# Kernel tuning notes

Measured on AMD Instinct MI355X. Metric: run time of the kernel, lower is better.

## Reference

```python
import jax, jax.numpy as jnp
import numpy as np

XN = 144
YN = 144
BN_EPS = 1e-5


def setup_inputs() -> dict:
    key = jax.random.key(0)
    k1, k2, k3, k4, k5 = jax.random.split(key, 5)
    B, P, M, F, C = 8, 12000, 32, 9, 64
    pillars = jax.random.normal(k1, (B, P, M, F), dtype=jnp.float32)
    pillar_indices = jax.random.randint(k2, (B, P, 3), 0, 144, dtype=jnp.int64)
    conv_w = jax.random.normal(k3, (C, F), dtype=jnp.float32) * 0.1  # 1x1 conv, no bias
    bn_gamma = jnp.ones((C,), dtype=jnp.float32)
    bn_beta = jnp.zeros((C,), dtype=jnp.float32)
    bn_mean = jax.random.normal(k4, (C,), dtype=jnp.float32) * 0.01
    bn_var = jax.random.uniform(k5, (C,), dtype=jnp.float32, minval=0.5, maxval=1.5)
    return {"pillars": pillars, "pillar_indices": pillar_indices, "conv_w": conv_w,
            "bn_gamma": bn_gamma, "bn_beta": bn_beta, "bn_mean": bn_mean, "bn_var": bn_var}


def reference(pillars, pillar_indices, conv_w, bn_gamma, bn_beta, bn_mean, bn_var):
    # pillars: [B, P, M, F] -> 1x1 conv over feature dim -> [B, C, P, M]
    x = jnp.einsum('bpmf,cf->bcpm', pillars, conv_w)
    # BatchNorm2d (inference) + ReLU
    inv_std = jax.lax.rsqrt(bn_var + BN_EPS)
    x = (x - bn_mean[None, :, None, None]) * (bn_gamma * inv_std)[None, :, None, None] \
        + bn_beta[None, :, None, None]
    x = jax.nn.relu(x)
    # MaxPool2d((1, M)): max over points-per-pillar axis -> [B, C, P]
    feat = jnp.max(x, axis=-1)
    # Scatter pillar features into BEV canvas [C, Xn*Yn]
    y_idx = pillar_indices[:, :, 1]                      # [B, P]
    x_idx = jnp.clip(pillar_indices[:, :, 2], 0, 143)    # [B, P]
    flat_idx = y_idx * XN + x_idx                        # [B, P]

    C = feat.shape[1]

    def scatter_one(f, idx):  # f: [C, P], idx: [P]
        canvas = jnp.zeros((C, XN * YN), dtype=f.dtype)
        return canvas.at[:, idx].set(f)

    out = jax.vmap(scatter_one)(feat, flat_idx)          # [B, C, Xn*Yn]
    return out.reshape(feat.shape[0], C, XN, YN)
```

## Files before the change

### kernel.cpp

```cpp
#include <hip/hip_runtime.h>
#include <hip/hip_bf16.h>
#include <stdint.h>

#define NB 8
#define NP 12000
#define NM 32
#define NF 9
#define NC 64
#define NX 144
#define NCELL (144*144)

#define PPW 8
#define FEAT_WAVES ((NB*NP)/PPW)
#define FEAT_BLOCKS (FEAT_WAVES/4)

typedef __attribute__((ext_vector_type(8)))  short bfrag8;
typedef __attribute__((ext_vector_type(16))) float accf16;
typedef float f32x4u __attribute__((ext_vector_type(4), aligned(4)));

#define WS_BTAB  0
#define WS_SHIFT 2048
#define WS_WIN   4096
#define WS_FEAT  668672
#define WS_NEED  (WS_FEAT + (size_t)NB*NP*NC*4)

__global__ void winner_prep_kernel(const int* __restrict__ idx, int* __restrict__ winner,
                                   const float* __restrict__ conv_w,
                                   const float* __restrict__ gamma,
                                   const float* __restrict__ beta,
                                   const float* __restrict__ mean,
                                   const float* __restrict__ var,
                                   unsigned short* __restrict__ btab,
                                   float* __restrict__ shift)
{
    int t = blockIdx.x * blockDim.x + threadIdx.x;
    if (t < NB * NP) {
        int b = t / NP;
        int p = t - b * NP;
        int y = idx[t * 3 + 1];
        int x = idx[t * 3 + 2];
        x = x < 0 ? 0 : (x > 143 ? 143 : x);
        y = y < 0 ? 0 : (y > 143 ? 143 : y);
        atomicMax(&winner[b * NCELL + y * NX + x], p);
    }
    if (blockIdx.x == 0) {
        int tt = threadIdx.x;
        if (tt < 128) {
            int ct = tt >> 6, L = tt & 63;
            int c  = ct * 32 + (L & 31);
            int kq = L >> 5;
            float sc = gamma[c] * rsqrtf(var[c] + 1e-5f);
            unsigned short* dst = btab + (ct * 64 + L) * 8;
            #pragma unroll
            for (int j = 0; j < 8; ++j) {
                int k = kq * 8 + j;
                float w = (k < NF) ? conv_w[c * NF + k] * sc : 0.f;
                __hip_bfloat16 h = __float2bfloat16(w);
                dst[j] = *(unsigned short*)&h;
            }
        }
        if (tt < NC) {
            float sc = gamma[tt] * rsqrtf(var[tt] + 1e-5f);
            shift[tt] = beta[tt] - mean[tt] * sc;
        }
    }
}

__device__ __forceinline__ float max16(const accf16& a) {
    float t0 = fmaxf(fmaxf(a[0], a[1]),  fmaxf(a[2], a[3]));
    float t1 = fmaxf(fmaxf(a[4], a[5]),  fmaxf(a[6], a[7]));
    float t2 = fmaxf(fmaxf(a[8], a[9]),  fmaxf(a[10], a[11]));
    float t3 = fmaxf(fmaxf(a[12], a[13]), fmaxf(a[14], a[15]));
    return fmaxf(fmaxf(t0, t1), fmaxf(t2, t3));
}

template <bool COMPACT>
__global__ void __launch_bounds__(256) feat_dense_kernel(
    const float* __restrict__ pillars,
    const unsigned short* __restrict__ btab,
    const float* __restrict__ shift,
    const int*   __restrict__ idx,
    const int*   __restrict__ winner,
    float* __restrict__ feat_ws,
    float* __restrict__ out)
{
    int tid  = threadIdx.x;
    int lane = tid & 63;
    int wave = blockIdx.x * 4 + (tid >> 6);
    int row  = lane & 31;
    int kq   = lane >> 5;

    bfrag8 b0 = *(const bfrag8*)(btab + lane * 8);
    bfrag8 b1 = *(const bfrag8*)(btab + (64 + lane) * 8);
    float  sh = shift[lane];
    accf16 z  = {};

    const float* wbase = pillars + (size_t)wave * (PPW * NM * NF) + row * NF;

    #pragma unroll
    for (int g = 0; g < PPW / 4; ++g) {
        f32x4u lo[4], hi[4];
        float  e8[4];
        #pragma unroll
        for (int i = 0; i < 4; ++i) {
            const float* base = wbase + (size_t)(g * 4 + i) * (NM * NF);
            lo[i] = *(const f32x4u*)(base);
            hi[i] = *(const f32x4u*)(base + 4);
            e8[i] = base[8];
        }
        #pragma unroll
        for (int i = 0; i < 4; ++i) {
            int pil = wave * PPW + g * 4 + i;
            float s[8];
            s[0] = kq ? e8[i] : lo[i][0];
            s[1] = kq ? 0.f   : lo[i][1];
            s[2] = kq ? 0.f   : lo[i][2];
            s[3] = kq ? 0.f   : lo[i][3];
            s[4] = kq ? 0.f   : hi[i][0];
            s[5] = kq ? 0.f   : hi[i][1];
            s[6] = kq ? 0.f   : hi[i][2];
            s[7] = kq ? 0.f   : hi[i][3];
            bfrag8 a;
            #pragma unroll
            for (int j = 0; j < 8; ++j) {
                __hip_bfloat16 h = __float2bfloat16(s[j]);
                a[j] = *(short*)&h;
            }
            accf16 acc0 = __builtin_amdgcn_mfma_f32_32x32x16_bf16(a, b0, z, 0, 0, 0);
            accf16 acc1 = __builtin_amdgcn_mfma_f32_32x32x16_bf16(a, b1, z, 0, 0, 0);

            float v0 = max16(acc0);
            float v1 = max16(acc1);
            v0 = fmaxf(v0, __shfl_xor(v0, 32));
            v1 = fmaxf(v1, __shfl_xor(v1, 32));
            float r = (lane < 32) ? v0 : v1;
            r += sh;
            r = r > 0.f ? r : 0.f;

            if (COMPACT) {
                feat_ws[(size_t)pil * NC + lane] = r;
            } else {
                int b = pil / NP, p = pil - b * NP;
                int y = idx[pil * 3 + 1], x = idx[pil * 3 + 2];
                x = x < 0 ? 0 : (x > 143 ? 143 : x);
                y = y < 0 ? 0 : (y > 143 ? 143 : y);
                int cell = y * NX + x;
                if (winner[b * NCELL + cell] == p)
                    out[((size_t)(b * NC + lane)) * NCELL + cell] = r;
            }
        }
    }
}

__global__ void __launch_bounds__(256) scatter_kernel(
    const int* __restrict__ winner,
    const float* __restrict__ feat_ws,
    float* __restrict__ out)
{
    int t  = blockIdx.x * blockDim.x + threadIdx.x;
    int c4 = t % (NCELL / 4);
    int bq = t / (NCELL / 4);
    int q  = bq & 3;
    int b  = bq >> 2;
    int cellbase = c4 * 4;

    int4 wv = *(const int4*)(winner + b * NCELL + cellbase);
    long long base0 = wv.x < 0 ? -1 : ((long long)(b * NP + wv.x)) * NC;
    long long base1 = wv.y < 0 ? -1 : ((long long)(b * NP + wv.y)) * NC;
    long long base2 = wv.z < 0 ? -1 : ((long long)(b * NP + wv.z)) * NC;
    long long base3 = wv.w < 0 ? -1 : ((long long)(b * NP + wv.w)) * NC;

    const float4 zf = make_float4(0.f, 0.f, 0.f, 0.f);
    #pragma unroll
    for (int k = 0; k < 4; ++k) {
        int c0 = q * 16 + k * 4;
        float4 f0 = base0 < 0 ? zf : *(const float4*)(feat_ws + base0 + c0);
        float4 f1 = base1 < 0 ? zf : *(const float4*)(feat_ws + base1 + c0);
        float4 f2 = base2 < 0 ? zf : *(const float4*)(feat_ws + base2 + c0);
        float4 f3 = base3 < 0 ? zf : *(const float4*)(feat_ws + base3 + c0);
        float* o = out + ((size_t)(b * NC + c0)) * NCELL + cellbase;
        *(float4*)(o + 0ULL * NCELL) = make_float4(f0.x, f1.x, f2.x, f3.x);
        *(float4*)(o + 1ULL * NCELL) = make_float4(f0.y, f1.y, f2.y, f3.y);
        *(float4*)(o + 2ULL * NCELL) = make_float4(f0.z, f1.z, f2.z, f3.z);
        *(float4*)(o + 3ULL * NCELL) = make_float4(f0.w, f1.w, f2.w, f3.w);
    }
}

extern "C" void kernel_launch(void* const* d_in, const int* in_sizes, int n_in,
                              void* d_out, int out_size, void* d_ws, size_t ws_size,
                              hipStream_t stream) {
    const float* pillars = (const float*)d_in[0];
    const int*   idx     = (const int*)d_in[1];
    const float* conv_w  = (const float*)d_in[2];
    const float* gamma   = (const float*)d_in[3];
    const float* beta    = (const float*)d_in[4];
    const float* mean    = (const float*)d_in[5];
    const float* var     = (const float*)d_in[6];
    float* out = (float*)d_out;

    char* ws = (char*)d_ws;
    unsigned short* btab    = (unsigned short*)(ws + WS_BTAB);
    float*          shift   = (float*)(ws + WS_SHIFT);
    int*            winner  = (int*)(ws + WS_WIN);
    float*          feat_ws = (float*)(ws + WS_FEAT);

    const bool compact = ws_size >= WS_NEED;

    hipMemsetAsync(winner, 0xFF, (size_t)NB * NCELL * sizeof(int), stream);
    winner_prep_kernel<<<(NB * NP + 255) / 256, 256, 0, stream>>>(
        idx, winner, conv_w, gamma, beta, mean, var, btab, shift);

    if (compact) {
        feat_dense_kernel<true><<<FEAT_BLOCKS, 256, 0, stream>>>(
            pillars, btab, shift, idx, winner, feat_ws, out);
        int sthreads = NB * 4 * (NCELL / 4);
        scatter_kernel<<<sthreads / 256, 256, 0, stream>>>(winner, feat_ws, out);
    } else {
        hipMemsetAsync(out, 0, (size_t)out_size * sizeof(float), stream);
        feat_dense_kernel<false><<<FEAT_BLOCKS, 256, 0, stream>>>(
            pillars, btab, shift, idx, winner, feat_ws, out);
    }
}
```

Before: 210.3 us.

## Store winner features in cell-major workspace and transpose via LDS in scatter

The feature kernel now writes only winning pillars' features, directly into a cell-indexed [B, cell, C] workspace instead of a pillar-indexed one. The winner check and cell index are hoisted to the start of each wave. The scatter kernel reads contiguous 64-cell tiles, transposes them through shared memory and writes coalesced rows of the [B, C, cell] output. This replaces the scattered gather by pillar id with streaming reads, at the cost of a larger workspace (cells x channels) and a possible fallback to the non-compact path if the workspace is too small.

```diff
diff --git a/kernel.cpp b/kernel.cpp
--- a/kernel.cpp
+++ b/kernel.cpp
@@ -13,6 +13,7 @@
 #define PPW 8
 #define FEAT_WAVES ((NB*NP)/PPW)
 #define FEAT_BLOCKS (FEAT_WAVES/4)
+#define TILES_PER_B (NCELL/64)
 
 typedef __attribute__((ext_vector_type(8)))  short bfrag8;
 typedef __attribute__((ext_vector_type(16))) float accf16;
@@ -21,8 +22,8 @@
 #define WS_BTAB  0
 #define WS_SHIFT 2048
 #define WS_WIN   4096
-#define WS_FEAT  668672
-#define WS_NEED  (WS_FEAT + (size_t)NB*NP*NC*4)
+#define WS_CELL  667648
+#define WS_NEED  (WS_CELL + (size_t)NB*NCELL*NC*4)
 
 __global__ void winner_prep_kernel(const int* __restrict__ idx, int* __restrict__ winner,
                                    const float* __restrict__ conv_w,
@@ -81,7 +82,7 @@
     const float* __restrict__ shift,
     const int*   __restrict__ idx,
     const int*   __restrict__ winner,
-    float* __restrict__ feat_ws,
+    float* __restrict__ feat_cell,
     float* __restrict__ out)
 {
     int tid  = threadIdx.x;
@@ -89,11 +90,26 @@
     int wave = blockIdx.x * 4 + (tid >> 6);
     int row  = lane & 31;
     int kq   = lane >> 5;
+    int b    = wave / (NP / PPW);
 
     bfrag8 b0 = *(const bfrag8*)(btab + lane * 8);
     bfrag8 b1 = *(const bfrag8*)(btab + (64 + lane) * 8);
     float  sh = shift[lane];
     accf16 z  = {};
+
+    int cellv[PPW];
+    bool winv[PPW];
+    #pragma unroll
+    for (int i = 0; i < PPW; ++i) {
+        int pil = wave * PPW + i;
+        int y = idx[pil * 3 + 1];
+        int x = idx[pil * 3 + 2];
+        x = x < 0 ? 0 : (x > 143 ? 143 : x);
+        y = y < 0 ? 0 : (y > 143 ? 143 : y);
+        int cell = y * NX + x;
+        cellv[i] = cell;
+        winv[i]  = (winner[b * NCELL + cell] == pil - b * NP);
+    }
 
     const float* wbase = pillars + (size_t)wave * (PPW * NM * NF) + row * NF;
 
@@ -110,7 +126,7 @@
         }
         #pragma unroll
         for (int i = 0; i < 4; ++i) {
-            int pil = wave * PPW + g * 4 + i;
+            int pi = g * 4 + i;
             float s[8];
             s[0] = kq ? e8[i] : lo[i][0];
             s[1] = kq ? 0.f   : lo[i][1];
@@ -137,52 +153,53 @@
             r += sh;
             r = r > 0.f ? r : 0.f;
 
-            if (COMPACT) {
-                feat_ws[(size_t)pil * NC + lane] = r;
-            } else {
-                int b = pil / NP, p = pil - b * NP;
-                int y = idx[pil * 3 + 1], x = idx[pil * 3 + 2];
-                x = x < 0 ? 0 : (x > 143 ? 143 : x);
-                y = y < 0 ? 0 : (y > 143 ? 143 : y);
-                int cell = y * NX + x;
-                if (winner[b * NCELL + cell] == p)
-                    out[((size_t)(b * NC + lane)) * NCELL + cell] = r;
+            if (winv[pi]) {
+                if (COMPACT) {
+                    feat_cell[((size_t)(b * NCELL + cellv[pi])) * NC + lane] = r;
+                } else {
+                    out[((size_t)(b * NC + lane)) * NCELL + cellv[pi]] = r;
+                }
             }
         }
     }
 }
 
-__global__ void __launch_bounds__(256) scatter_kernel(
+__global__ void __launch_bounds__(256) scatter_t_kernel(
     const int* __restrict__ winner,
-    const float* __restrict__ feat_ws,
+    const float* __restrict__ feat_cell,
     float* __restrict__ out)
 {
-    int t  = blockIdx.x * blockDim.x + threadIdx.x;
-    int c4 = t % (NCELL / 4);
-    int bq = t / (NCELL / 4);
-    int q  = bq & 3;
-    int b  = bq >> 2;
-    int cellbase = c4 * 4;
-
-    int4 wv = *(const int4*)(winner + b * NCELL + cellbase);
-    long long base0 = wv.x < 0 ? -1 : ((long long)(b * NP + wv.x)) * NC;
-    long long base1 = wv.y < 0 ? -1 : ((long long)(b * NP + wv.y)) * NC;
-    long long base2 = wv.z < 0 ? -1 : ((long long)(b * NP + wv.z)) * NC;
-    long long base3 = wv.w < 0 ? -1 : ((long long)(b * NP + wv.w)) * NC;
-
-    const float4 zf = make_float4(0.f, 0.f, 0.f, 0.f);
-    #pragma unroll
-    for (int k = 0; k < 4; ++k) {
-        int c0 = q * 16 + k * 4;
-        float4 f0 = base0 < 0 ? zf : *(const float4*)(feat_ws + base0 + c0);
-        float4 f1 = base1 < 0 ? zf : *(const float4*)(feat_ws + base1 + c0);
-        float4 f2 = base2 < 0 ? zf : *(const float4*)(feat_ws + base2 + c0);
-        float4 f3 = base3 < 0 ? zf : *(const float4*)(feat_ws + base3 + c0);
-        float* o = out + ((size_t)(b * NC + c0)) * NCELL + cellbase;
-        *(float4*)(o + 0ULL * NCELL) = make_float4(f0.x, f1.x, f2.x, f3.x);
-        *(float4*)(o + 1ULL * NCELL) = make_float4(f0.y, f1.y, f2.y, f3.y);
-        *(float4*)(o + 2ULL * NCELL) = make_float4(f0.z, f1.z, f2.z, f3.z);
-        *(float4*)(o + 3ULL * NCELL) = make_float4(f0.w, f1.w, f2.w, f3.w);
+    __shared__ float ld[NC * 68];
+    int tile = blockIdx.x;
+    int b    = tile / TILES_PER_B;
+    int cb   = (tile - b * TILES_PER_B) * 64;
+    int t    = threadIdx.x;
+
+    {
+        int cell = t >> 2, q = t & 3;
+        int w = winner[b * NCELL + cb + cell];
+        const f32x4u* src = (const f32x4u*)(feat_cell +
+                             ((size_t)(b * NCELL + cb + cell)) * NC);
+        #pragma unroll
+        for (int k = 0; k < 4; ++k) {
+            f32x4u v = {0.f, 0.f, 0.f, 0.f};
+            if (w >= 0) v = src[q * 4 + k];
+            int c = q * 16 + k * 4;
+            ld[(c + 0) * 68 + cell] = v[0];
+            ld[(c + 1) * 68 + cell] = v[1];
+            ld[(c + 2) * 68 + cell] = v[2];
+            ld[(c + 3) * 68 + cell] = v[3];
+        }
+    }
+    __syncthreads();
+    {
+        int c = t >> 2, qq = t & 3;
+        float* o = out + ((size_t)(b * NC + c)) * NCELL + cb + qq * 16;
+        const float* lrow = ld + c * 68 + qq * 16;
+        #pragma unroll
+        for (int k = 0; k < 4; ++k) {
+            *(f32x4u*)(o + k * 4) = *(const f32x4u*)(lrow + k * 4);
+        }
     }
 }
 
@@ -199,10 +216,10 @@
     float* out = (float*)d_out;
 
     char* ws = (char*)d_ws;
-    unsigned short* btab    = (unsigned short*)(ws + WS_BTAB);
-    float*          shift   = (float*)(ws + WS_SHIFT);
-    int*            winner  = (int*)(ws + WS_WIN);
-    float*          feat_ws = (float*)(ws + WS_FEAT);
+    unsigned short* btab      = (unsigned short*)(ws + WS_BTAB);
+    float*          shift     = (float*)(ws + WS_SHIFT);
+    int*            winner    = (int*)(ws + WS_WIN);
+    float*          feat_cell = (float*)(ws + WS_CELL);
 
     const bool compact = ws_size >= WS_NEED;
 
@@ -212,12 +229,12 @@
 
     if (compact) {
         feat_dense_kernel<true><<<FEAT_BLOCKS, 256, 0, stream>>>(
-            pillars, btab, shift, idx, winner, feat_ws, out);
-        int sthreads = NB * 4 * (NCELL / 4);
-        scatter_kernel<<<sthreads / 256, 256, 0, stream>>>(winner, feat_ws, out);
+            pillars, btab, shift, idx, winner, feat_cell, out);
+        scatter_t_kernel<<<NB * TILES_PER_B, 256, 0, stream>>>(
+            winner, feat_cell, out);
     } else {
         hipMemsetAsync(out, 0, (size_t)out_size * sizeof(float), stream);
         feat_dense_kernel<false><<<FEAT_BLOCKS, 256, 0, stream>>>(
-            pillars, btab, shift, idx, winner, feat_ws, out);
-    }
-}
+            pillars, btab, shift, idx, winner, feat_cell, out);
+    }
+}
```

Result: no change. 208.7 us (-0.8%).
